# Kernel optimization log

Hardware: AMD Instinct MI355X
Metric: run time of the kernel (lower is better)

## Reference

```python
import jax, jax.numpy as jnp
import numpy as np

B, L, C, H = 8, 16384, 128, 4
EPS = 1e-5


def setup_inputs() -> dict:
    key = jax.random.key(0)
    k1, k2, k3, k4 = jax.random.split(key, 4)
    return {
        "x": jax.random.normal(k1, (B, L, C), dtype=jnp.float32),
        "W_qkv": jax.random.normal(k2, (3 * C, C), dtype=jnp.float32) * (C ** -0.5),
        "W_out": jax.random.normal(k3, (C, C), dtype=jnp.float32) * (C ** -0.5),
        "b_out": jax.random.normal(k4, (C,), dtype=jnp.float32) * 0.01,
        "gn_w": jnp.ones((C,), dtype=jnp.float32),
        "gn_b": jnp.zeros((C,), dtype=jnp.float32),
    }


def reference(x, W_qkv, W_out, b_out, gn_w, gn_b):
    b, l, c = x.shape
    h = H
    d = c // h                      # dim_head
    scale = d ** -0.5
    xc = jnp.swapaxes(x, 1, 2)      # [b, c, l]
    # 1x1 conv == channel matmul
    qkv = jnp.einsum('oc,bcl->bol', W_qkv, xc)     # [b, 3c, l]
    q, k, v = jnp.split(qkv, 3, axis=1)
    q = q.reshape(b, h, d, l)
    k = k.reshape(b, h, d, l)
    v = v.reshape(b, h, d, l)
    q = jax.nn.softmax(q, axis=2) * scale          # softmax over head-dim
    k = jax.nn.softmax(k, axis=3)                  # softmax over length
    context = jnp.einsum('bhcj,bhdj->bhcd', k, v)  # [b, h, d, d]
    out = jnp.einsum('bhcd,bhdi->bhci', context, q)  # [b, h, d, l]
    out = out.reshape(b, h * d, l)
    out = jnp.einsum('oc,bcl->bol', W_out, out) + b_out[None, :, None]
    # GroupNorm(1, c): normalize over (channel, length) per sample
    mean = jnp.mean(out, axis=(1, 2), keepdims=True)
    var = jnp.var(out, axis=(1, 2), keepdims=True)
    out = (out - mean) * jax.lax.rsqrt(var + EPS)
    out = out * gn_w[None, :, None] + gn_b[None, :, None]
    return jnp.swapaxes(out, 1, 2)                 # [b, l, c]
```

## Files before the change

kernel.cpp:

```cpp
#include <hip/hip_runtime.h>

#define BATCH 8
#define SEQL 16384
#define NCH 128
#define NH 4
#define HD 32
#define GEPS 1e-5f

typedef __bf16 bf16x8 __attribute__((ext_vector_type(8)));
typedef __bf16 bf16x4 __attribute__((ext_vector_type(4)));
typedef float f32x4 __attribute__((ext_vector_type(4)));

#define WKV_B   0
#define WQ_B    65536
#define WO_B    98304
#define CTXB_B  131072
#define CTXF_B  196608
#define ZF_B    327680
#define GNS_B   331776
#define GNF_B   331840
#define ZERO_BYTES (131072 + 4096 + 64 + 64)

__global__ void k_prep(const float* __restrict__ wqkv, const float* __restrict__ wout,
                       char* __restrict__ wsb) {
    int i = blockIdx.x * 256 + threadIdx.x;
    __bf16* wkvb = (__bf16*)(wsb + WKV_B);
    __bf16* wqb  = (__bf16*)(wsb + WQ_B);
    __bf16* wob  = (__bf16*)(wsb + WO_B);
    if (i < 384 * 128) {
        int o = i >> 7, c = i & 127;
        __bf16 v = (__bf16)wqkv[i];
        if (o < 128) wqb[o * 128 + c] = v;
        else         wkvb[(o - 128) * 128 + c] = v;
    }
    if (i < 128 * 128) wob[i] = (__bf16)wout[i];
}

__global__ __launch_bounds__(256, 3) void k_pass1(const float* __restrict__ x,
                                                  char* __restrict__ wsb) {
    __shared__ __attribute__((aligned(16))) __bf16 xb[8352];
    __shared__ __attribute__((aligned(16))) __bf16 ekv[16464];
    const int t = threadIdx.x;
    const int lane = t & 63, wave = t >> 6;
    const int n16 = lane & 15, q = lane >> 4;
    const int batch = blockIdx.x >> 7, sub = blockIdx.x & 127;
    const __bf16* __restrict__ wkvb = (const __bf16*)(wsb + WKV_B);

    f32x4 ctxacc[2][2];
#pragma unroll
    for (int i = 0; i < 2; i++)
#pragma unroll
        for (int j = 0; j < 2; j++) ctxacc[i][j] = (f32x4){0.f, 0.f, 0.f, 0.f};
    float zacc[4][4];
#pragma unroll
    for (int i = 0; i < 4; i++)
#pragma unroll
        for (int j = 0; j < 4; j++) zacc[i][j] = 0.f;

    for (int rep = 0; rep < 2; rep++) {
        const int chunk = sub + rep * 128;
        const float* xg = x + (size_t)(batch * SEQL + chunk * 64) * NCH;
        __syncthreads();
#pragma unroll
        for (int r = 0; r < 8; r++) {
            int e = t + r * 256;
            int tok = e >> 5, c4 = (e & 31) * 4;
            float4 v = ((const float4*)xg)[e];
            bf16x4 h; h.x = (__bf16)v.x; h.y = (__bf16)v.y; h.z = (__bf16)v.z; h.w = (__bf16)v.w;
            *(bf16x4*)&xb[(c4 >> 5) * 2088 + ((c4 >> 3) & 3) * 520 + tok * 8 + (c4 & 7)] = h;
        }
        __syncthreads();
        f32x4 kvacc[4][4];
#pragma unroll
        for (int i = 0; i < 4; i++)
#pragma unroll
            for (int j = 0; j < 4; j++) kvacc[i][j] = (f32x4){0.f, 0.f, 0.f, 0.f};
#pragma unroll
        for (int ks = 0; ks < 4; ks++) {
            bf16x8 awk[4];
#pragma unroll
            for (int mt = 0; mt < 4; mt++)
                awk[mt] = *(const bf16x8*)&wkvb[(wave * 64 + mt * 16 + n16) * 128 + ks * 32 + q * 8];
            bf16x8 b[4];
#pragma unroll
            for (int nt = 0; nt < 4; nt++)
                b[nt] = *(const bf16x8*)&xb[ks * 2088 + q * 520 + (nt * 16 + n16) * 8];
#pragma unroll
            for (int mt = 0; mt < 4; mt++)
#pragma unroll
                for (int nt = 0; nt < 4; nt++)
                    kvacc[mt][nt] = __builtin_amdgcn_mfma_f32_16x16x32_bf16(
                        awk[mt], b[nt], kvacc[mt][nt], 0, 0, 0);
        }
#pragma unroll
        for (int mt = 0; mt < 4; mt++)
#pragma unroll
            for (int nt = 0; nt < 4; nt++) {
                int tt = nt * 16 + n16;
                int base = (tt >> 5) * 8232 + ((tt >> 3) & 3) * 2056 + (tt & 7);
#pragma unroll
                for (int r = 0; r < 4; r++) {
                    float vv = kvacc[mt][nt][r];
                    if (wave < 2) { vv = __expf(vv); zacc[mt][r] += vv; }
                    int o = wave * 64 + mt * 16 + q * 4 + r;
                    ekv[base + o * 8] = (__bf16)vv;
                }
            }
        __syncthreads();
#pragma unroll
        for (int ks2 = 0; ks2 < 2; ks2++) {
            bf16x8 ea[2], vb[2];
#pragma unroll
            for (int ml = 0; ml < 2; ml++) {
                ea[ml] = *(const bf16x8*)&ekv[ks2 * 8232 + q * 2056 + (wave * 32 + ml * 16 + n16) * 8];
                vb[ml] = *(const bf16x8*)&ekv[ks2 * 8232 + q * 2056 + (128 + wave * 32 + ml * 16 + n16) * 8];
            }
#pragma unroll
            for (int ml = 0; ml < 2; ml++)
#pragma unroll
                for (int nl = 0; nl < 2; nl++)
                    ctxacc[ml][nl] = __builtin_amdgcn_mfma_f32_16x16x32_bf16(
                        ea[ml], vb[nl], ctxacc[ml][nl], 0, 0, 0);
        }
    }
    float* ctxf = (float*)(wsb + CTXF_B) + ((size_t)(batch * 4 + wave) * 32) * 32;
#pragma unroll
    for (int ml = 0; ml < 2; ml++)
#pragma unroll
        for (int nl = 0; nl < 2; nl++)
#pragma unroll
            for (int r = 0; r < 4; r++)
                atomicAdd(&ctxf[(ml * 16 + q * 4 + r) * 32 + nl * 16 + n16], ctxacc[ml][nl][r]);
    if (wave < 2) {
        float* Zf = (float*)(wsb + ZF_B) + batch * 128;
#pragma unroll
        for (int mt = 0; mt < 4; mt++)
#pragma unroll
            for (int r = 0; r < 4; r++) {
                float z = zacc[mt][r];
                z += __shfl_xor(z, 1); z += __shfl_xor(z, 2);
                z += __shfl_xor(z, 4); z += __shfl_xor(z, 8);
                if (n16 == 0) atomicAdd(&Zf[wave * 64 + mt * 16 + q * 4 + r], z);
            }
    }
}

__global__ void k_ctxnorm(char* __restrict__ wsb) {
    int i = blockIdx.x * 256 + threadIdx.x;
    if (i < BATCH * NH * HD * HD) {
        const float* ctxf = (const float*)(wsb + CTXF_B);
        const float* Zf = (const float*)(wsb + ZF_B);
        __bf16* ctxb = (__bf16*)(wsb + CTXB_B);
        int c = (i >> 5) & 31, h = (i >> 10) & 3, b = i >> 12;
        ctxb[i] = (__bf16)(ctxf[i] / Zf[b * 128 + h * 32 + c]);
    }
}

__global__ __launch_bounds__(256, 4) void k_pass2(const float* __restrict__ x,
                                                  const float* __restrict__ bout,
                                                  char* __restrict__ wsb,
                                                  float* __restrict__ out) {
    __shared__ __attribute__((aligned(16))) __bf16 bufA[8352];
    __shared__ __attribute__((aligned(16))) __bf16 bufB[8352];
    __shared__ float gred[8];
    const int t = threadIdx.x;
    const int lane = t & 63, wave = t >> 6;
    const int n16 = lane & 15, q = lane >> 4;
    const int batch = blockIdx.x >> 8, chunk = blockIdx.x & 255;
    const __bf16* __restrict__ wqb = (const __bf16*)(wsb + WQ_B);
    const __bf16* __restrict__ wob = (const __bf16*)(wsb + WO_B);
    const __bf16* __restrict__ ctxb = (const __bf16*)(wsb + CTXB_B);

    const size_t tok0 = (size_t)batch * SEQL + chunk * 64;
    const float* xg = x + tok0 * NCH;
#pragma unroll
    for (int r = 0; r < 8; r++) {
        int e = t + r * 256;
        int tok = e >> 5, c4 = (e & 31) * 4;
        float4 v = ((const float4*)xg)[e];
        bf16x4 h; h.x = (__bf16)v.x; h.y = (__bf16)v.y; h.z = (__bf16)v.z; h.w = (__bf16)v.w;
        *(bf16x4*)&bufA[(c4 >> 5) * 2088 + ((c4 >> 3) & 3) * 520 + tok * 8 + (c4 & 7)] = h;
    }
    bf16x8 aq[2][4];
#pragma unroll
    for (int ml = 0; ml < 2; ml++)
#pragma unroll
        for (int ks = 0; ks < 4; ks++)
            aq[ml][ks] = *(const bf16x8*)&wqb[(wave * 32 + ml * 16 + n16) * 128 + ks * 32 + q * 8];
    bf16x8 actx[2];
#pragma unroll
    for (int ml = 0; ml < 2; ml++)
        actx[ml] = *(const bf16x8*)&ctxb[((size_t)(batch * 4 + wave) * 32 + ml * 16 + n16) * 32 + q * 8];
    __syncthreads();

    f32x4 qacc[2][4];
#pragma unroll
    for (int i = 0; i < 2; i++)
#pragma unroll
        for (int j = 0; j < 4; j++) qacc[i][j] = (f32x4){0.f, 0.f, 0.f, 0.f};
#pragma unroll
    for (int ks = 0; ks < 4; ks++) {
        bf16x8 b[4];
#pragma unroll
        for (int nt = 0; nt < 4; nt++)
            b[nt] = *(const bf16x8*)&bufA[ks * 2088 + q * 520 + (nt * 16 + n16) * 8];
#pragma unroll
        for (int ml = 0; ml < 2; ml++)
#pragma unroll
            for (int nt = 0; nt < 4; nt++)
                qacc[ml][nt] = __builtin_amdgcn_mfma_f32_16x16x32_bf16(
                    aq[ml][ks], b[nt], qacc[ml][nt], 0, 0, 0);
    }
#pragma unroll
    for (int nt = 0; nt < 4; nt++) {
        float ss = 0.f;
#pragma unroll
        for (int ml = 0; ml < 2; ml++)
#pragma unroll
            for (int r = 0; r < 4; r++) {
                float e = __expf(qacc[ml][nt][r]);
                qacc[ml][nt][r] = e;
                ss += e;
            }
        ss += __shfl_xor(ss, 16);
        ss += __shfl_xor(ss, 32);
        float inv = 0.17677669529663687f / ss;
#pragma unroll
        for (int ml = 0; ml < 2; ml++)
#pragma unroll
            for (int r = 0; r < 4; r++) qacc[ml][nt][r] *= inv;
    }
    __syncthreads();
#pragma unroll
    for (int ml = 0; ml < 2; ml++)
#pragma unroll
        for (int nt = 0; nt < 4; nt++) {
            bf16x4 h;
            h.x = (__bf16)qacc[ml][nt][0]; h.y = (__bf16)qacc[ml][nt][1];
            h.z = (__bf16)qacc[ml][nt][2]; h.w = (__bf16)qacc[ml][nt][3];
            *(bf16x4*)&bufB[wave * 2088 + (ml * 2 + (q >> 1)) * 520 +
                            (nt * 16 + n16) * 8 + (q & 1) * 4] = h;
        }
    __builtin_amdgcn_fence(__ATOMIC_ACQ_REL, "workgroup");
#pragma unroll
    for (int ml = 0; ml < 2; ml++)
#pragma unroll
        for (int nt = 0; nt < 4; nt++) {
            bf16x8 pb = *(const bf16x8*)&bufB[wave * 2088 + q * 520 + (nt * 16 + n16) * 8];
            f32x4 aacc = __builtin_amdgcn_mfma_f32_16x16x32_bf16(
                actx[ml], pb, (f32x4){0.f, 0.f, 0.f, 0.f}, 0, 0, 0);
            bf16x4 h;
            h.x = (__bf16)aacc[0]; h.y = (__bf16)aacc[1];
            h.z = (__bf16)aacc[2]; h.w = (__bf16)aacc[3];
            *(bf16x4*)&bufA[wave * 2088 + (ml * 2 + (q >> 1)) * 520 +
                            (nt * 16 + n16) * 8 + (q & 1) * 4] = h;
        }
    __syncthreads();
    f32x4 oacc[2][4];
#pragma unroll
    for (int i = 0; i < 2; i++)
#pragma unroll
        for (int j = 0; j < 4; j++) oacc[i][j] = (f32x4){0.f, 0.f, 0.f, 0.f};
#pragma unroll
    for (int ks = 0; ks < 4; ks++) {
        bf16x8 ao = *(const bf16x8*)&wob[(wave * 32 + 0 * 16 + n16) * 128 + ks * 32 + q * 8];
        bf16x8 ao1 = *(const bf16x8*)&wob[(wave * 32 + 1 * 16 + n16) * 128 + ks * 32 + q * 8];
        bf16x8 b[4];
#pragma unroll
        for (int nt = 0; nt < 4; nt++)
            b[nt] = *(const bf16x8*)&bufA[ks * 2088 + q * 520 + (nt * 16 + n16) * 8];
#pragma unroll
        for (int nt = 0; nt < 4; nt++) {
            oacc[0][nt] = __builtin_amdgcn_mfma_f32_16x16x32_bf16(ao, b[nt], oacc[0][nt], 0, 0, 0);
            oacc[1][nt] = __builtin_amdgcn_mfma_f32_16x16x32_bf16(ao1, b[nt], oacc[1][nt], 0, 0, 0);
        }
    }
    float4 bias[2];
#pragma unroll
    for (int ml = 0; ml < 2; ml++)
        bias[ml] = *(const float4*)&bout[wave * 32 + ml * 16 + q * 4];
    float s1 = 0.f, s2 = 0.f;
#pragma unroll
    for (int ml = 0; ml < 2; ml++)
#pragma unroll
        for (int nt = 0; nt < 4; nt++) {
            float4 vv;
            vv.x = oacc[ml][nt][0] + bias[ml].x;
            vv.y = oacc[ml][nt][1] + bias[ml].y;
            vv.z = oacc[ml][nt][2] + bias[ml].z;
            vv.w = oacc[ml][nt][3] + bias[ml].w;
            s1 += vv.x + vv.y + vv.z + vv.w;
            s2 += vv.x * vv.x + vv.y * vv.y + vv.z * vv.z + vv.w * vv.w;
            *(float4*)&out[(tok0 + nt * 16 + n16) * NCH + wave * 32 + ml * 16 + q * 4] = vv;
        }
#pragma unroll
    for (int off = 32; off > 0; off >>= 1) {
        s1 += __shfl_xor(s1, off);
        s2 += __shfl_xor(s2, off);
    }
    if (lane == 0) { gred[wave] = s1; gred[4 + wave] = s2; }
    __syncthreads();
    if (t == 0) {
        float* gns = (float*)(wsb + GNS_B);
        atomicAdd(&gns[batch * 2 + 0], gred[0] + gred[1] + gred[2] + gred[3]);
        atomicAdd(&gns[batch * 2 + 1], gred[4] + gred[5] + gred[6] + gred[7]);
    }
}

__global__ void k_gnfinal(char* __restrict__ wsb) {
    int b = threadIdx.x;
    if (b < BATCH) {
        const float n = (float)NCH * (float)SEQL;
        const float* gns = (const float*)(wsb + GNS_B);
        float* gnf = (float*)(wsb + GNF_B);
        float mean = gns[b * 2] / n;
        float var = gns[b * 2 + 1] / n - mean * mean;
        gnf[b * 2] = mean;
        gnf[b * 2 + 1] = rsqrtf(var + GEPS);
    }
}

__global__ __launch_bounds__(256) void k_gnorm(float* __restrict__ out,
                                               const char* __restrict__ wsb,
                                               const float* __restrict__ gw,
                                               const float* __restrict__ gb) {
    size_t i4 = (size_t)blockIdx.x * 256 + threadIdx.x;
    int b = (int)(i4 >> 19);
    int c4 = (int)(i4 & 31);
    const float* gnf = (const float*)(wsb + GNF_B);
    float mean = gnf[b * 2], rstd = gnf[b * 2 + 1];
    float4 w = *(const float4*)&gw[c4 * 4];
    float4 bb = *(const float4*)&gb[c4 * 4];
    float4 v = ((float4*)out)[i4];
    v.x = (v.x - mean) * rstd * w.x + bb.x;
    v.y = (v.y - mean) * rstd * w.y + bb.y;
    v.z = (v.z - mean) * rstd * w.z + bb.z;
    v.w = (v.w - mean) * rstd * w.w + bb.w;
    ((float4*)out)[i4] = v;
}

extern "C" void kernel_launch(void* const* d_in, const int* in_sizes, int n_in,
                              void* d_out, int out_size, void* d_ws, size_t ws_size,
                              hipStream_t stream) {
    const float* x    = (const float*)d_in[0];
    const float* wqkv = (const float*)d_in[1];
    const float* wout = (const float*)d_in[2];
    const float* bout = (const float*)d_in[3];
    const float* gw   = (const float*)d_in[4];
    const float* gb   = (const float*)d_in[5];
    float* out = (float*)d_out;
    char* wsb  = (char*)d_ws;

    hipMemsetAsync(wsb + CTXF_B, 0, ZERO_BYTES, stream);
    k_prep<<<192, 256, 0, stream>>>(wqkv, wout, wsb);
    k_pass1<<<1024, 256, 0, stream>>>(x, wsb);
    k_ctxnorm<<<128, 256, 0, stream>>>(wsb);
    k_pass2<<<2048, 256, 0, stream>>>(x, bout, wsb, out);
    k_gnfinal<<<1, 64, 0, stream>>>(wsb);
    k_gnorm<<<16384, 256, 0, stream>>>(out, wsb, gw, gb);
}
```

Baseline: 282.3 us.

## Load x straight into registers in pass1 and replace atomics with partial-sum reduction

Pass1 now loads x directly from global memory into MFMA operand registers, with the token dimension as the A operand, so the LDS staging buffer and its barrier are gone. The next chunk's x is prefetched while the current one computes. The context and Z atomics are replaced by per-block partial writes (context in bf16), which a new k_reduce kernel sums. This also removes the large memset and raises the occupancy target to 4. In exchange it writes about 10 MB of partials, runs a serial 32-block reduction, and rounds the partial contexts to bf16.

```diff
diff --git a/kernel.cpp b/kernel.cpp
--- a/kernel.cpp
+++ b/kernel.cpp
@@ -15,11 +15,10 @@
 #define WQ_B    65536
 #define WO_B    98304
 #define CTXB_B  131072
-#define CTXF_B  196608
-#define ZF_B    327680
-#define GNS_B   331776
-#define GNF_B   331840
-#define ZERO_BYTES (131072 + 4096 + 64 + 64)
+#define CTXP_B  196608
+#define ZP_B    (196608 + 8388608)
+#define GNS_B   (ZP_B + 2097152)
+#define GNF_B   (GNS_B + 64)
 
 __global__ void k_prep(const float* __restrict__ wqkv, const float* __restrict__ wout,
                        char* __restrict__ wsb) {
@@ -36,14 +35,14 @@
     if (i < 128 * 128) wob[i] = (__bf16)wout[i];
 }
 
-__global__ __launch_bounds__(256, 3) void k_pass1(const float* __restrict__ x,
+__global__ __launch_bounds__(256, 4) void k_pass1(const float* __restrict__ x,
                                                   char* __restrict__ wsb) {
-    __shared__ __attribute__((aligned(16))) __bf16 xb[8352];
-    __shared__ __attribute__((aligned(16))) __bf16 ekv[16464];
+    __shared__ __attribute__((aligned(16))) __bf16 ekv[256 * 68];
     const int t = threadIdx.x;
     const int lane = t & 63, wave = t >> 6;
     const int n16 = lane & 15, q = lane >> 4;
-    const int batch = blockIdx.x >> 7, sub = blockIdx.x & 127;
+    const int blk = blockIdx.x;
+    const int batch = blk >> 7, sub = blk & 127;
     const __bf16* __restrict__ wkvb = (const __bf16*)(wsb + WKV_B);
 
     f32x4 ctxacc[2][2];
@@ -51,69 +50,76 @@
     for (int i = 0; i < 2; i++)
 #pragma unroll
         for (int j = 0; j < 2; j++) ctxacc[i][j] = (f32x4){0.f, 0.f, 0.f, 0.f};
-    float zacc[4][4];
-#pragma unroll
-    for (int i = 0; i < 4; i++)
-#pragma unroll
-        for (int j = 0; j < 4; j++) zacc[i][j] = 0.f;
+    float zacc[8];
+#pragma unroll
+    for (int j = 0; j < 8; j++) zacc[j] = 0.f;
+
+    float4 px[8];
+    {
+        const float* xr = x + ((size_t)(batch * SEQL + sub * 64) + wave * 16 + n16) * NCH;
+#pragma unroll
+        for (int ks = 0; ks < 4; ks++) {
+            px[2 * ks]     = *(const float4*)&xr[ks * 32 + q * 8];
+            px[2 * ks + 1] = *(const float4*)&xr[ks * 32 + q * 8 + 4];
+        }
+    }
 
     for (int rep = 0; rep < 2; rep++) {
-        const int chunk = sub + rep * 128;
-        const float* xg = x + (size_t)(batch * SEQL + chunk * 64) * NCH;
-        __syncthreads();
-#pragma unroll
-        for (int r = 0; r < 8; r++) {
-            int e = t + r * 256;
-            int tok = e >> 5, c4 = (e & 31) * 4;
-            float4 v = ((const float4*)xg)[e];
-            bf16x4 h; h.x = (__bf16)v.x; h.y = (__bf16)v.y; h.z = (__bf16)v.z; h.w = (__bf16)v.w;
-            *(bf16x4*)&xb[(c4 >> 5) * 2088 + ((c4 >> 3) & 3) * 520 + tok * 8 + (c4 & 7)] = h;
-        }
-        __syncthreads();
-        f32x4 kvacc[4][4];
-#pragma unroll
-        for (int i = 0; i < 4; i++)
-#pragma unroll
-            for (int j = 0; j < 4; j++) kvacc[i][j] = (f32x4){0.f, 0.f, 0.f, 0.f};
+        bf16x8 ax[4];
 #pragma unroll
         for (int ks = 0; ks < 4; ks++) {
-            bf16x8 awk[4];
-#pragma unroll
-            for (int mt = 0; mt < 4; mt++)
-                awk[mt] = *(const bf16x8*)&wkvb[(wave * 64 + mt * 16 + n16) * 128 + ks * 32 + q * 8];
-            bf16x8 b[4];
-#pragma unroll
-            for (int nt = 0; nt < 4; nt++)
-                b[nt] = *(const bf16x8*)&xb[ks * 2088 + q * 520 + (nt * 16 + n16) * 8];
-#pragma unroll
-            for (int mt = 0; mt < 4; mt++)
-#pragma unroll
-                for (int nt = 0; nt < 4; nt++)
-                    kvacc[mt][nt] = __builtin_amdgcn_mfma_f32_16x16x32_bf16(
-                        awk[mt], b[nt], kvacc[mt][nt], 0, 0, 0);
-        }
-#pragma unroll
-        for (int mt = 0; mt < 4; mt++)
-#pragma unroll
-            for (int nt = 0; nt < 4; nt++) {
-                int tt = nt * 16 + n16;
-                int base = (tt >> 5) * 8232 + ((tt >> 3) & 3) * 2056 + (tt & 7);
-#pragma unroll
-                for (int r = 0; r < 4; r++) {
-                    float vv = kvacc[mt][nt][r];
-                    if (wave < 2) { vv = __expf(vv); zacc[mt][r] += vv; }
-                    int o = wave * 64 + mt * 16 + q * 4 + r;
-                    ekv[base + o * 8] = (__bf16)vv;
+            bf16x8 a;
+            a[0] = (__bf16)px[2 * ks].x;     a[1] = (__bf16)px[2 * ks].y;
+            a[2] = (__bf16)px[2 * ks].z;     a[3] = (__bf16)px[2 * ks].w;
+            a[4] = (__bf16)px[2 * ks + 1].x; a[5] = (__bf16)px[2 * ks + 1].y;
+            a[6] = (__bf16)px[2 * ks + 1].z; a[7] = (__bf16)px[2 * ks + 1].w;
+            ax[ks] = a;
+        }
+#pragma unroll
+        for (int half = 0; half < 2; half++) {
+            f32x4 acc[8];
+#pragma unroll
+            for (int j = 0; j < 8; j++) acc[j] = (f32x4){0.f, 0.f, 0.f, 0.f};
+#pragma unroll
+            for (int ks = 0; ks < 4; ks++) {
+#pragma unroll
+                for (int j = 0; j < 8; j++) {
+                    int o = (half * 8 + j) * 16 + n16;
+                    bf16x8 bw = *(const bf16x8*)&wkvb[o * 128 + ks * 32 + q * 8];
+                    acc[j] = __builtin_amdgcn_mfma_f32_16x16x32_bf16(ax[ks], bw, acc[j], 0, 0, 0);
                 }
             }
+#pragma unroll
+            for (int j = 0; j < 8; j++) {
+                int o = (half * 8 + j) * 16 + n16;
+                f32x4 v = acc[j];
+                if (half == 0) {
+                    v[0] = __expf(v[0]); v[1] = __expf(v[1]);
+                    v[2] = __expf(v[2]); v[3] = __expf(v[3]);
+                    zacc[j] += v[0] + v[1] + v[2] + v[3];
+                }
+                bf16x4 hh;
+                hh.x = (__bf16)v[0]; hh.y = (__bf16)v[1];
+                hh.z = (__bf16)v[2]; hh.w = (__bf16)v[3];
+                *(bf16x4*)&ekv[o * 68 + wave * 16 + q * 4] = hh;
+            }
+        }
+        if (rep == 0) {
+            const float* xr = x + ((size_t)(batch * SEQL + (sub + 128) * 64) + wave * 16 + n16) * NCH;
+#pragma unroll
+            for (int ks = 0; ks < 4; ks++) {
+                px[2 * ks]     = *(const float4*)&xr[ks * 32 + q * 8];
+                px[2 * ks + 1] = *(const float4*)&xr[ks * 32 + q * 8 + 4];
+            }
+        }
         __syncthreads();
 #pragma unroll
         for (int ks2 = 0; ks2 < 2; ks2++) {
             bf16x8 ea[2], vb[2];
 #pragma unroll
             for (int ml = 0; ml < 2; ml++) {
-                ea[ml] = *(const bf16x8*)&ekv[ks2 * 8232 + q * 2056 + (wave * 32 + ml * 16 + n16) * 8];
-                vb[ml] = *(const bf16x8*)&ekv[ks2 * 8232 + q * 2056 + (128 + wave * 32 + ml * 16 + n16) * 8];
+                ea[ml] = *(const bf16x8*)&ekv[(wave * 32 + ml * 16 + n16) * 68 + ks2 * 32 + q * 8];
+                vb[ml] = *(const bf16x8*)&ekv[(128 + wave * 32 + ml * 16 + n16) * 68 + ks2 * 32 + q * 8];
             }
 #pragma unroll
             for (int ml = 0; ml < 2; ml++)
@@ -122,38 +128,64 @@
                     ctxacc[ml][nl] = __builtin_amdgcn_mfma_f32_16x16x32_bf16(
                         ea[ml], vb[nl], ctxacc[ml][nl], 0, 0, 0);
         }
-    }
-    float* ctxf = (float*)(wsb + CTXF_B) + ((size_t)(batch * 4 + wave) * 32) * 32;
-#pragma unroll
-    for (int ml = 0; ml < 2; ml++)
-#pragma unroll
-        for (int nl = 0; nl < 2; nl++)
-#pragma unroll
-            for (int r = 0; r < 4; r++)
-                atomicAdd(&ctxf[(ml * 16 + q * 4 + r) * 32 + nl * 16 + n16], ctxacc[ml][nl][r]);
-    if (wave < 2) {
-        float* Zf = (float*)(wsb + ZF_B) + batch * 128;
-#pragma unroll
-        for (int mt = 0; mt < 4; mt++)
-#pragma unroll
-            for (int r = 0; r < 4; r++) {
-                float z = zacc[mt][r];
-                z += __shfl_xor(z, 1); z += __shfl_xor(z, 2);
-                z += __shfl_xor(z, 4); z += __shfl_xor(z, 8);
-                if (n16 == 0) atomicAdd(&Zf[wave * 64 + mt * 16 + q * 4 + r], z);
-            }
-    }
-}
-
-__global__ void k_ctxnorm(char* __restrict__ wsb) {
-    int i = blockIdx.x * 256 + threadIdx.x;
-    if (i < BATCH * NH * HD * HD) {
-        const float* ctxf = (const float*)(wsb + CTXF_B);
-        const float* Zf = (const float*)(wsb + ZF_B);
-        __bf16* ctxb = (__bf16*)(wsb + CTXB_B);
-        int c = (i >> 5) & 31, h = (i >> 10) & 3, b = i >> 12;
-        ctxb[i] = (__bf16)(ctxf[i] / Zf[b * 128 + h * 32 + c]);
-    }
+        if (rep == 0) __syncthreads();
+    }
+    __bf16* ctxp = (__bf16*)(wsb + CTXP_B) + ((size_t)blk * 4 + wave) * 1024;
+#pragma unroll
+    for (int ml = 0; ml < 2; ml++)
+#pragma unroll
+        for (int nl = 0; nl < 2; nl++) {
+            bf16x4 hh;
+            hh.x = (__bf16)ctxacc[ml][nl][0]; hh.y = (__bf16)ctxacc[ml][nl][1];
+            hh.z = (__bf16)ctxacc[ml][nl][2]; hh.w = (__bf16)ctxacc[ml][nl][3];
+            *(bf16x4*)&ctxp[(nl * 16 + n16) * 32 + ml * 16 + q * 4] = hh;
+        }
+    float* zp = (float*)(wsb + ZP_B) + ((size_t)blk * 4 + wave) * 128;
+#pragma unroll
+    for (int j = 0; j < 8; j++) {
+        float z = zacc[j];
+        z += __shfl_xor(z, 16);
+        z += __shfl_xor(z, 32);
+        if (q == 0) zp[j * 16 + n16] = z;
+    }
+}
+
+__global__ __launch_bounds__(256) void k_reduce(char* __restrict__ wsb) {
+    __shared__ float zpart[8][32];
+    __shared__ float zs[32];
+    const int t = threadIdx.x;
+    const int b = blockIdx.x >> 2, h = blockIdx.x & 3;
+    const float* zp = (const float*)(wsb + ZP_B);
+    {
+        int c = t & 31, g = t >> 5;
+        float s = 0.f;
+        for (int s8 = g; s8 < 128; s8 += 8)
+#pragma unroll
+            for (int w = 0; w < 4; w++)
+                s += zp[((size_t)(b * 128 + s8) * 4 + w) * 128 + h * 32 + c];
+        zpart[g][c] = s;
+    }
+    __syncthreads();
+    if (t < 32) {
+        float s = 0.f;
+#pragma unroll
+        for (int g = 0; g < 8; g++) s += zpart[g][t];
+        zs[t] = s;
+    }
+    __syncthreads();
+    const __bf16* ctxp = (const __bf16*)(wsb + CTXP_B);
+    float s0 = 0.f, s1 = 0.f, s2 = 0.f, s3 = 0.f;
+    size_t base = ((size_t)(b * 512 + h)) * 1024 + t * 4;
+    for (int sub = 0; sub < 128; sub++) {
+        bf16x4 v = *(const bf16x4*)&ctxp[base + (size_t)sub * 4096];
+        s0 += (float)v.x; s1 += (float)v.y; s2 += (float)v.z; s3 += (float)v.w;
+    }
+    int d = t >> 3, c0 = (t & 7) * 4;
+    __bf16* ctxb = (__bf16*)(wsb + CTXB_B) + (size_t)(b * 4 + h) * 1024;
+    ctxb[(c0 + 0) * 32 + d] = (__bf16)(s0 / zs[c0 + 0]);
+    ctxb[(c0 + 1) * 32 + d] = (__bf16)(s1 / zs[c0 + 1]);
+    ctxb[(c0 + 2) * 32 + d] = (__bf16)(s2 / zs[c0 + 2]);
+    ctxb[(c0 + 3) * 32 + d] = (__bf16)(s3 / zs[c0 + 3]);
 }
 
 __global__ __launch_bounds__(256, 4) void k_pass2(const float* __restrict__ x,
@@ -263,8 +295,8 @@
         for (int j = 0; j < 4; j++) oacc[i][j] = (f32x4){0.f, 0.f, 0.f, 0.f};
 #pragma unroll
     for (int ks = 0; ks < 4; ks++) {
-        bf16x8 ao = *(const bf16x8*)&wob[(wave * 32 + 0 * 16 + n16) * 128 + ks * 32 + q * 8];
-        bf16x8 ao1 = *(const bf16x8*)&wob[(wave * 32 + 1 * 16 + n16) * 128 + ks * 32 + q * 8];
+        bf16x8 ao  = *(const bf16x8*)&wob[(wave * 32 + n16) * 128 + ks * 32 + q * 8];
+        bf16x8 ao1 = *(const bf16x8*)&wob[(wave * 32 + 16 + n16) * 128 + ks * 32 + q * 8];
         bf16x8 b[4];
 #pragma unroll
         for (int nt = 0; nt < 4; nt++)
@@ -351,10 +383,10 @@
     float* out = (float*)d_out;
     char* wsb  = (char*)d_ws;
 
-    hipMemsetAsync(wsb + CTXF_B, 0, ZERO_BYTES, stream);
+    hipMemsetAsync(wsb + GNS_B, 0, 64, stream);
     k_prep<<<192, 256, 0, stream>>>(wqkv, wout, wsb);
     k_pass1<<<1024, 256, 0, stream>>>(x, wsb);
-    k_ctxnorm<<<128, 256, 0, stream>>>(wsb);
+    k_reduce<<<32, 256, 0, stream>>>(wsb);
     k_pass2<<<2048, 256, 0, stream>>>(x, bout, wsb, out);
     k_gnfinal<<<1, 64, 0, stream>>>(wsb);
     k_gnorm<<<16384, 256, 0, stream>>>(out, wsb, gw, gb);
```

Result: no change. 286.9 us (+1.6%).
